# Performance work log

Hardware: AMD Instinct MI355X
Metric: run time of the kernel (lower is better)

## Reference

```python
import jax, jax.numpy as jnp
import numpy as np

EPS = 1e-6


def _make_window_masks(nhw, nww, ws, shift):
    ph = jnp.arange(nhw).reshape(nhw, 1, 1, 1, 1, 1)
    pw = jnp.arange(nww).reshape(1, nww, 1, 1, 1, 1)
    qh = jnp.arange(ws).reshape(1, 1, ws, 1, 1, 1)
    qw = jnp.arange(ws).reshape(1, 1, 1, ws, 1, 1)
    kh = jnp.arange(ws).reshape(1, 1, 1, 1, ws, 1)
    kw = jnp.arange(ws).reshape(1, 1, 1, 1, 1, ws)
    top = ph == 0
    left = pw == 0
    qa = qh < shift
    ka = kh < shift
    ql = qw < shift
    kl = kw < shift
    m = ((left & top & (ql == kl) & (qa == ka))
         | (left & ~top & (ql == kl))
         | (~left & top & (qa == ka))
         | (~left & ~top))
    m = jnp.broadcast_to(m, (nhw, nww, ws, ws, ws, ws))
    return m.reshape(nhw, nww, ws * ws, ws * ws)


def _window(ws, x):
    # x: [b, nh, H, W, e] -> [b, nh, H//ws, W//ws, ws, ws, e]
    b, nh, H, W, e = x.shape
    x = x.reshape(b, nh, H // ws, ws, W // ws, ws, e)
    return jnp.transpose(x, (0, 1, 2, 4, 3, 5, 6))


def _unwindow(x):
    b, nh, h, w, wh, ww, e = x.shape
    x = jnp.transpose(x, (0, 1, 2, 4, 3, 5, 6))
    return x.reshape(b, nh, h * wh, w * ww, e)


def _rope_theta(pos, n_heads, d_head):
    # AxialRoPE: dim = d_head // 2, freqs [n_heads, dim//4]
    dim = d_head // 2
    freqs = jnp.exp(jnp.linspace(np.float32(np.log(np.pi)), np.float32(np.log(10.0 * np.pi)), n_heads * dim // 4 + 1)[:-1])
    freqs = freqs.reshape(dim // 4, n_heads).T  # [nh, dim//4]
    th = pos[..., None, 0:1] * freqs  # [b,H,W,nh,dim//4]
    tw = pos[..., None, 1:2] * freqs
    theta = jnp.concatenate([th, tw], axis=-1)  # [b,H,W,nh,d_head//4]
    return jnp.moveaxis(theta, -2, -4)  # [b,nh,H,W,d_head//4]


def _apply_rope(x, theta):
    # rotates first 2*d of head dim, pairs (i, i+d); rest passes through
    d = theta.shape[-1]
    x1, x2, rest = x[..., :d], x[..., d:2 * d], x[..., 2 * d:]
    cos, sin = jnp.cos(theta), jnp.sin(theta)
    y1 = x1 * cos - x2 * sin
    y2 = x2 * cos + x1 * sin
    return jnp.concatenate([y1, y2, rest], axis=-1)


def _forward(x, pos, cond, norm_scale, mod_w, mod_b, qkv_w, attn_scale, out_w, window_size, window_shift):
    b, H, W, d_model = x.shape
    n_heads = attn_scale.shape[0]
    d_head = d_model // n_heads
    ws, shift = window_size, window_shift
    skip = x
    # adaLN modulation: SiLU -> Linear(cond_features, 3*d_model)
    c = jax.nn.silu(cond) @ mod_w.T + mod_b  # [b, 3*d_model]
    sh, sc, gate = jnp.split(c, 3, axis=-1)
    # RMSNorm
    ms = jnp.mean(jnp.square(x.astype(jnp.float32)), axis=-1, keepdims=True)
    xn = x * (norm_scale * jax.lax.rsqrt(ms + EPS)).astype(x.dtype)
    # modulate
    xn = xn * (1.0 + sc[:, None, None, :]) + sh[:, None, None, :]
    # qkv projection: rearrange 'n h w (t nh e) -> t n nh h w e'
    qkv = (xn @ qkv_w.T).reshape(b, H, W, 3, n_heads, d_head)
    qkv = jnp.transpose(qkv, (3, 0, 4, 1, 2, 5))  # [3,b,nh,H,W,e]
    q, k, v = qkv[0], qkv[1], qkv[2]
    # cosine-sim QK scaling (per-head learned scale, eps 1e-6)
    sqrt_s = jnp.sqrt(attn_scale)[:, None, None, None]
    q = q * (sqrt_s * jax.lax.rsqrt(jnp.sum(jnp.square(q), -1, keepdims=True) + EPS))
    k = k * (sqrt_s * jax.lax.rsqrt(jnp.sum(jnp.square(k), -1, keepdims=True) + EPS))
    # axial RoPE
    theta = _rope_theta(pos, n_heads, d_head)
    q = _apply_rope(q, theta)
    k = _apply_rope(k, theta)
    # shifted-window attention with sdpa scale = 1.0
    def shift_win(t):
        return _window(ws, jnp.roll(t, (shift, shift), axis=(-3, -2)))
    h, w = H // ws, W // ws
    L = ws * ws
    qs = shift_win(q).reshape(b, n_heads, h, w, L, d_head)
    ks = shift_win(k).reshape(b, n_heads, h, w, L, d_head)
    vs = shift_win(v).reshape(b, n_heads, h, w, L, d_head)
    mask = _make_window_masks(h, w, ws, shift)  # [h,w,L,L] bool
    scores = jnp.einsum('bnhwqe,bnhwke->bnhwqk', qs, ks)
    scores = jnp.where(mask, scores, jnp.asarray(-1e9, scores.dtype))
    attn = jax.nn.softmax(scores, axis=-1)
    o = jnp.einsum('bnhwqk,bnhwke->bnhwqe', attn, vs)
    o = o.reshape(b, n_heads, h, w, ws, ws, d_head)
    o = jnp.roll(_unwindow(o), (-shift, -shift), axis=(-3, -2))  # [b,nh,H,W,e]
    o = jnp.transpose(o, (0, 2, 3, 1, 4)).reshape(b, H, W, d_model)
    o = o @ out_w.T
    return skip + gate[:, None, None, :] * o


def setup_inputs() -> dict:
    key = jax.random.key(0)
    ks = jax.random.split(key, 6)
    B, H, W, D, NH, CF = 2, 256, 256, 256, 4, 768
    x = jax.random.normal(ks[0], (B, H, W, D), jnp.float32)
    hh = jnp.linspace(-1.0, 1.0, H)
    ww = jnp.linspace(-1.0, 1.0, W)
    pos = jnp.stack(jnp.meshgrid(hh, ww, indexing='ij'), axis=-1)  # [H,W,2]
    pos = jnp.broadcast_to(pos, (B, H, W, 2)).astype(jnp.float32)
    cond = jax.random.normal(ks[1], (B, CF), jnp.float32)
    norm_scale = jnp.ones((D,), jnp.float32)
    mod_w = jax.random.normal(ks[2], (3 * D, CF), jnp.float32) * 0.02
    mod_b = jnp.zeros((3 * D,), jnp.float32)
    qkv_w = jax.random.normal(ks[3], (3 * D, D), jnp.float32) * (D ** -0.5)
    attn_scale = jnp.full((NH,), 10.0, jnp.float32)
    out_w = jax.random.normal(ks[4], (D, D), jnp.float32) * (D ** -0.5)
    return {"x": x, "pos": pos, "cond": cond, "norm_scale": norm_scale,
            "mod_w": mod_w, "mod_b": mod_b, "qkv_w": qkv_w,
            "attn_scale": attn_scale, "out_w": out_w,
            "window_size": 8, "window_shift": 4}


def reference(x, pos, cond, norm_scale, mod_w, mod_b, qkv_w, attn_scale, out_w, window_size, window_shift):
    return _forward(x, pos, cond, norm_scale, mod_w, mod_b, qkv_w, attn_scale, out_w, window_size, window_shift)
```

## Files before the change

### kernel.cpp

```cpp
#include <hip/hip_runtime.h>
#include <hip/hip_bf16.h>
#include <cstdint>

#define DEV __device__ __forceinline__

constexpr int D_   = 256;
constexpr int CF_  = 768;
constexpr int NTOK = 131072;
constexpr int SHIFT = 4;
constexpr float EPS_ = 1e-6f;

typedef short bf16x8 __attribute__((ext_vector_type(8)));
typedef float f32x4  __attribute__((ext_vector_type(4)));

DEV float bf2f(unsigned short u) {
    unsigned v = ((unsigned)u) << 16;
    return __builtin_bit_cast(float, v);
}
DEV unsigned short f2bf(float f) {
    unsigned u = __builtin_bit_cast(unsigned, f);
    unsigned r = (u + 0x7fffu + ((u >> 16) & 1u)) >> 16;
    return (unsigned short)r;
}
DEV unsigned cvtpk(float lo, float hi) {
    unsigned r;
    asm("v_cvt_pk_bf16_f32 %0, %1, %2" : "=v"(r) : "v"(lo), "v"(hi));
    return r;
}
DEV float wave_sum(float v) {
    #pragma unroll
    for (int o = 32; o; o >>= 1) v += __shfl_xor(v, o, 64);
    return v;
}
DEV void gl_lds16(const void* g, void* l) {
    __builtin_amdgcn_global_load_lds(
        (const __attribute__((address_space(1))) void*)g,
        (__attribute__((address_space(3))) void*)l, 16, 0, 0);
}

__global__ void k_mod(const float* __restrict__ cond, const float* __restrict__ mod_w,
                      const float* __restrict__ mod_b, float* __restrict__ c) {
    int wv = threadIdx.x >> 6, lane = threadIdx.x & 63;
    int idx = blockIdx.x * 4 + wv;
    int b = idx / (3 * D_), j = idx % (3 * D_);
    float acc = 0.f;
    for (int k = lane; k < CF_; k += 64) {
        float cv = cond[b * CF_ + k];
        float s = cv / (1.f + expf(-cv));
        acc += s * mod_w[(size_t)j * CF_ + k];
    }
    acc = wave_sum(acc);
    if (lane == 0) c[b * (3 * D_) + j] = acc + mod_b[j];
}

__global__ void k_prep(const float* __restrict__ x, const float* __restrict__ c,
                       const float* __restrict__ norm_scale,
                       const float* __restrict__ qkv_w, const float* __restrict__ out_w,
                       unsigned short* __restrict__ xnb,
                       unsigned short* __restrict__ qkvwb, unsigned short* __restrict__ outwb) {
    if (blockIdx.x < 32768) {
        int wv = threadIdx.x >> 6, lane = threadIdx.x & 63;
        int t = blockIdx.x * 4 + wv;
        int b = t >> 16;
        const float* xp = x + (size_t)t * D_ + lane * 4;
        float4 v = *(const float4*)xp;
        float s = v.x * v.x + v.y * v.y + v.z * v.z + v.w * v.w;
        s = wave_sum(s);
        float rinv = rsqrtf(s * (1.f / D_) + EPS_);
        float4 sc = *(const float4*)(c + b * 768 + 256 + lane * 4);
        float4 sh = *(const float4*)(c + b * 768 + lane * 4);
        float4 ns = *(const float4*)(norm_scale + lane * 4);
        float y0 = v.x * rinv * ((1.f + sc.x) * ns.x) + sh.x;
        float y1 = v.y * rinv * ((1.f + sc.y) * ns.y) + sh.y;
        float y2 = v.z * rinv * ((1.f + sc.z) * ns.z) + sh.z;
        float y3 = v.w * rinv * ((1.f + sc.w) * ns.w) + sh.w;
        uint2 p;
        p.x = cvtpk(y0, y1);
        p.y = cvtpk(y2, y3);
        *(uint2*)(xnb + (size_t)t * D_ + lane * 4) = p;
    } else {
        int i = (blockIdx.x - 32768) * 256 + threadIdx.x;
        const float* src; unsigned short* dst; int off;
        if (i < 49152) { src = qkv_w; dst = qkvwb; off = i * 4; }
        else           { src = out_w; dst = outwb; off = (i - 49152) * 4; }
        float4 v = *(const float4*)(src + off);
        uint2 p;
        p.x = cvtpk(v.x, v.y);
        p.y = cvtpk(v.z, v.w);
        *(uint2*)(dst + off) = p;
    }
}

__global__ __launch_bounds__(256) void k_qkv_mfma(const unsigned short* __restrict__ xnb,
                                                  const unsigned short* __restrict__ wb,
                                                  const float* __restrict__ attn_scale,
                                                  unsigned short* __restrict__ qkv) {
    __shared__ unsigned short As[2][128 * 32];
    __shared__ unsigned short Bs[2][128 * 32];
    const int t = threadIdx.x, l = t & 63, w = t >> 6;
    const int bid = blockIdx.x;
    const int lid = (bid & 7) * 768 + (bid >> 3);
    const int m0 = (lid / 6) * 128;
    const int nt = lid % 6;
    const int n0 = nt * 128;
    const int wm = w >> 1, wn = w & 1;
    f32x4 acc[4][4] = {};

    const int srow = w * 32 + (l >> 2);
    const int scol = (l & 3) * 8;
    const unsigned short* aA = xnb + (size_t)(m0 + srow) * 256 + scol;
    const unsigned short* aB = wb  + (size_t)(n0 + srow) * 256 + scol;

    auto stage = [&](int buf, int k0) {
        gl_lds16(aA + k0,            &As[buf][(w * 2 + 0) * 512]);
        gl_lds16(aA + k0 + 16 * 256, &As[buf][(w * 2 + 1) * 512]);
        gl_lds16(aB + k0,            &Bs[buf][(w * 2 + 0) * 512]);
        gl_lds16(aB + k0 + 16 * 256, &Bs[buf][(w * 2 + 1) * 512]);
    };

    stage(0, 0);
    __syncthreads();
    int cur = 0;
    #pragma unroll
    for (int step = 0; step < 8; ++step) {
        if (step < 7) stage(cur ^ 1, (step + 1) * 32);
        bf16x8 af[4], bff[4];
        #pragma unroll
        for (int i = 0; i < 4; i++) {
            af[i]  = *(const bf16x8*)&As[cur][(wm * 64 + i * 16 + (l & 15)) * 32 + (l >> 4) * 8];
            bff[i] = *(const bf16x8*)&Bs[cur][(wn * 64 + i * 16 + (l & 15)) * 32 + (l >> 4) * 8];
        }
        #pragma unroll
        for (int i = 0; i < 4; i++)
            #pragma unroll
            for (int j = 0; j < 4; j++)
                acc[i][j] = __builtin_amdgcn_mfma_f32_16x16x32_bf16(af[i], bff[j], acc[i][j], 0, 0, 0);
        __syncthreads();
        cur ^= 1;
    }

    const int row0 = m0 + wm * 64 + (l >> 4) * 4;
    const int col0 = n0 + wn * 64 + (l & 15);
    const int q16 = l & 15;

    if (nt < 4) {
        const int head = (nt * 2 + wn) & 3;
        const float ssc = sqrtf(attn_scale[head]);
        const float freq = expf(1.14472988584940017f + (float)((q16 & 7) * 4 + head) * 0.07195578545544534f);
        #pragma unroll
        for (int i = 0; i < 4; i++) {
            #pragma unroll
            for (int rg = 0; rg < 4; rg++) {
                float ss = acc[i][0][rg] * acc[i][0][rg] + acc[i][1][rg] * acc[i][1][rg]
                         + acc[i][2][rg] * acc[i][2][rg] + acc[i][3][rg] * acc[i][3][rg];
                ss += __shfl_xor(ss, 1, 64);
                ss += __shfl_xor(ss, 2, 64);
                ss += __shfl_xor(ss, 4, 64);
                ss += __shfl_xor(ss, 8, 64);
                const float rinv = ssc * rsqrtf(ss + EPS_);
                const int row = row0 + i * 16 + rg;
                const int oy = (row >> 8) & 255, ox = row & 255;
                const float ph = -1.f + (float)oy * (2.f / 255.f);
                const float pw = -1.f + (float)ox * (2.f / 255.f);
                const float th = ((q16 < 8) ? ph : pw) * freq;
                float sn, cs;
                __sincosf(th, &sn, &cs);
                const float n0v = acc[i][0][rg] * rinv;
                const float n1v = acc[i][1][rg] * rinv;
                const float n2v = acc[i][2][rg] * rinv;
                const float n3v = acc[i][3][rg] * rinv;
                unsigned short* qp = qkv + (size_t)row * 768 + col0;
                qp[0]  = f2bf(n0v * cs - n1v * sn);
                qp[16] = f2bf(n1v * cs + n0v * sn);
                qp[32] = f2bf(n2v);
                qp[48] = f2bf(n3v);
            }
        }
    } else {
        #pragma unroll
        for (int i = 0; i < 4; i++)
            #pragma unroll
            for (int j = 0; j < 4; j++) {
                #pragma unroll
                for (int rg = 0; rg < 4; rg++)
                    qkv[(size_t)(row0 + i * 16 + rg) * 768 + col0 + j * 16] = f2bf(acc[i][j][rg]);
            }
    }
}

__global__ __launch_bounds__(256) void k_attn_out(const unsigned short* __restrict__ qkv,
                                                  const unsigned short* __restrict__ outwb,
                                                  const float* __restrict__ x,
                                                  const float* __restrict__ c,
                                                  float* __restrict__ out) {
    __shared__ unsigned short Mem[4 * 64 * 72];
    __shared__ float Ls[4][64];
    const int w = threadIdx.x >> 6, l = threadIdx.x & 63;
    const int bid = blockIdx.x;
    const int lid = (bid & 7) * 256 + (bid >> 3);
    const int wx = lid & 31, wy = (lid >> 5) & 31, b = lid >> 10;
    const int head = w;
    const int g = l >> 4, q16 = l & 15;
    unsigned short* Vt = &Mem[w * 4608];

    auto tokof = [&](int p) -> size_t {
        int oy = (wy * 8 + (p >> 3) - SHIFT) & 255;
        int ox = (wx * 8 + (p & 7) - SHIFT) & 255;
        return (size_t)b * 65536 + (size_t)oy * 256 + ox;
    };

    {
        const unsigned short* vp = qkv + tokof(l) * 768 + 512 + head * 64;
        uint4 vr[8];
        #pragma unroll
        for (int i = 0; i < 8; i++) vr[i] = *(const uint4*)(vp + i * 8);
        #pragma unroll
        for (int i = 0; i < 8; i++) {
            unsigned wd[4] = {vr[i].x, vr[i].y, vr[i].z, vr[i].w};
            #pragma unroll
            for (int cc = 0; cc < 4; cc++) {
                Vt[(i * 8 + cc * 2 + 0) * 72 + l] = (unsigned short)(wd[cc] & 0xffff);
                Vt[(i * 8 + cc * 2 + 1) * 72 + l] = (unsigned short)(wd[cc] >> 16);
            }
        }
    }

    bf16x8 af[4][2], bq[4][2];
    #pragma unroll
    for (int i = 0; i < 4; i++) {
        size_t tk = tokof(i * 16 + q16);
        const unsigned short* kp = qkv + tk * 768 + 256 + head * 64 + g * 8;
        af[i][0] = *(const bf16x8*)(kp);
        af[i][1] = *(const bf16x8*)(kp + 32);
        const unsigned short* qp = qkv + tk * 768 + head * 64 + g * 8;
        bq[i][0] = *(const bf16x8*)(qp);
        bq[i][1] = *(const bf16x8*)(qp + 32);
    }

    f32x4 st[4][4] = {};
    #pragma unroll
    for (int ks = 0; ks < 2; ks++)
        #pragma unroll
        for (int i = 0; i < 4; i++)
            #pragma unroll
            for (int j = 0; j < 4; j++)
                st[i][j] = __builtin_amdgcn_mfma_f32_16x16x32_bf16(af[i][ks], bq[j][ks], st[i][j], 0, 0, 0);

    const bool topw = (wy == 0), leftw = (wx == 0);
    if (topw || leftw) {
        #pragma unroll
        for (int j = 0; j < 4; j++) {
            int query = 16 * j + q16;
            bool qa = ((query >> 3) < 4), qlf = ((query & 7) < 4);
            #pragma unroll
            for (int i = 0; i < 4; i++)
                #pragma unroll
                for (int r = 0; r < 4; r++) {
                    int key = 16 * i + 4 * g + r;
                    bool ok = (!leftw || (qlf == ((key & 7) < 4))) &&
                              (!topw || (qa == ((key >> 3) < 4)));
                    if (!ok) st[i][j][r] = -1e9f;
                }
        }
    }

    #pragma unroll
    for (int j = 0; j < 4; j++) {
        float m = -1e30f;
        #pragma unroll
        for (int i = 0; i < 4; i++)
            #pragma unroll
            for (int r = 0; r < 4; r++) m = fmaxf(m, st[i][j][r]);
        m = fmaxf(m, __shfl_xor(m, 16, 64));
        m = fmaxf(m, __shfl_xor(m, 32, 64));
        float s = 0.f;
        #pragma unroll
        for (int i = 0; i < 4; i++)
            #pragma unroll
            for (int r = 0; r < 4; r++) {
                float p = __expf(st[i][j][r] - m);
                st[i][j][r] = p;
                s += p;
            }
        s += __shfl_xor(s, 16, 64);
        s += __shfl_xor(s, 32, 64);
        if (g == 0) Ls[w][16 * j + q16] = s;
    }
    __syncthreads();

    bf16x8 vb[4][2];
    #pragma unroll
    for (int j = 0; j < 4; j++) {
        vb[j][0] = *(const bf16x8*)&Vt[(16 * j + q16) * 72 + g * 8];
        vb[j][1] = *(const bf16x8*)&Vt[(16 * j + q16) * 72 + 32 + g * 8];
    }
    const int ghi = g >> 1;
    const int srcl0 = ((2 * (g & 1)) & 3) * 16 + q16;
    const int srcl1 = ((2 * (g & 1) + 1) & 3) * 16 + q16;
    f32x4 o[4][4] = {};
    #pragma unroll
    for (int qb = 0; qb < 4; qb++) {
        unsigned pk[8];
        #pragma unroll
        for (int ih = 0; ih < 4; ih++) {
            pk[2 * ih]     = cvtpk(st[ih][qb][0], st[ih][qb][1]);
            pk[2 * ih + 1] = cvtpk(st[ih][qb][2], st[ih][qb][3]);
        }
        unsigned pw[8];
        #pragma unroll
        for (int ks = 0; ks < 2; ks++) {
            #pragma unroll
            for (int wd = 0; wd < 4; wd++) {
                const int srcl = (wd < 2) ? srcl0 : srcl1;
                unsigned va  = (unsigned)__shfl((int)pk[4 * ks + (wd & 1)], srcl, 64);
                unsigned vbb = (unsigned)__shfl((int)pk[4 * ks + 2 + (wd & 1)], srcl, 64);
                pw[ks * 4 + wd] = ghi ? vbb : va;
            }
        }
        uint4 paw0 = {pw[0], pw[1], pw[2], pw[3]};
        uint4 paw1 = {pw[4], pw[5], pw[6], pw[7]};
        bf16x8 paA = __builtin_bit_cast(bf16x8, paw0);
        bf16x8 paB = __builtin_bit_cast(bf16x8, paw1);
        #pragma unroll
        for (int j = 0; j < 4; j++) {
            o[qb][j] = __builtin_amdgcn_mfma_f32_16x16x32_bf16(paA, vb[j][0], o[qb][j], 0, 0, 0);
            o[qb][j] = __builtin_amdgcn_mfma_f32_16x16x32_bf16(paB, vb[j][1], o[qb][j], 0, 0, 0);
        }
    }

    __syncthreads();
    unsigned short* ost = Mem;
    #pragma unroll
    for (int i = 0; i < 4; i++) {
        float4 lv = *(const float4*)&Ls[w][16 * i + 4 * g];
        float lvr[4] = {lv.x, lv.y, lv.z, lv.w};
        #pragma unroll
        for (int r = 0; r < 4; r++) {
            const float invl = 1.f / lvr[r];
            const int row = 16 * i + 4 * g + r;
            #pragma unroll
            for (int j = 0; j < 4; j++)
                ost[row * 264 + head * 64 + 16 * j + q16] = f2bf(o[i][j][r] * invl);
        }
    }
    __syncthreads();

    f32x4 acc2[4][4] = {};
    #pragma unroll
    for (int ks = 0; ks < 8; ks++) {
        bf16x8 a2[4], b2[4];
        #pragma unroll
        for (int i = 0; i < 4; i++)
            a2[i] = *(const bf16x8*)&ost[(16 * i + q16) * 264 + ks * 32 + g * 8];
        #pragma unroll
        for (int j = 0; j < 4; j++)
            b2[j] = *(const bf16x8*)&outwb[(size_t)(w * 64 + 16 * j + q16) * 256 + ks * 32 + g * 8];
        #pragma unroll
        for (int i = 0; i < 4; i++)
            #pragma unroll
            for (int j = 0; j < 4; j++)
                acc2[i][j] = __builtin_amdgcn_mfma_f32_16x16x32_bf16(a2[i], b2[j], acc2[i][j], 0, 0, 0);
    }

    float gates[4];
    #pragma unroll
    for (int j = 0; j < 4; j++) gates[j] = c[b * 768 + 512 + w * 64 + 16 * j + q16];
    #pragma unroll
    for (int i = 0; i < 4; i++) {
        #pragma unroll
        for (int r = 0; r < 4; r++) {
            const int row = 16 * i + 4 * g + r;
            const size_t tok = tokof(row);
            float* op = out + tok * 256 + w * 64 + q16;
            const float* xp = x + tok * 256 + w * 64 + q16;
            #pragma unroll
            for (int j = 0; j < 4; j++)
                op[16 * j] = xp[16 * j] + gates[j] * acc2[i][j][r];
        }
    }
}

extern "C" void kernel_launch(void* const* d_in, const int* in_sizes, int n_in,
                              void* d_out, int out_size, void* d_ws, size_t ws_size,
                              hipStream_t stream) {
    const float* x          = (const float*)d_in[0];
    const float* cond       = (const float*)d_in[2];
    const float* norm_scale = (const float*)d_in[3];
    const float* mod_w      = (const float*)d_in[4];
    const float* mod_b      = (const float*)d_in[5];
    const float* qkv_w      = (const float*)d_in[6];
    const float* attn_scale = (const float*)d_in[7];
    const float* out_w      = (const float*)d_in[8];

    char* ws = (char*)d_ws;
    float* c               = (float*)ws;
    unsigned short* xnb    = (unsigned short*)(ws + 8192);
    unsigned short* qkvwb  = (unsigned short*)(ws + 8192 + 67108864);
    unsigned short* outwb  = (unsigned short*)(ws + 8192 + 67108864 + 393216);
    unsigned short* qkv    = (unsigned short*)(ws + 8192 + 67108864 + 524288);
    float* out             = (float*)d_out;

    hipLaunchKernelGGL(k_mod,  dim3(384),   dim3(256), 0, stream, cond, mod_w, mod_b, c);
    hipLaunchKernelGGL(k_prep, dim3(33024), dim3(256), 0, stream,
                       x, c, norm_scale, qkv_w, out_w, xnb, qkvwb, outwb);
    hipLaunchKernelGGL(k_qkv_mfma, dim3(6144), dim3(256), 0, stream, xnb, qkvwb, attn_scale, qkv);
    hipLaunchKernelGGL(k_attn_out, dim3(2048), dim3(256), 0, stream, qkv, outwb, x, c, out);
}
```

Baseline: 286.2 us.

## Swizzle QKV GEMM LDS tiles and stage epilogue through LDS for coalesced stores

The QKV GEMM kernel now XOR-swizzles the k-column slot of its LDS A/B tiles, on both the global-to-LDS staging side and the fragment read side, to reduce bank conflicts. The epilogue no longer writes scattered 2-byte bf16 values straight to global memory. It writes the 128x128 output tile into a padded LDS buffer, synchronises, and then each thread stores 16-byte vectors along contiguous rows. The goal is to turn uncoalesced global writes into full-width stores, at the cost of an extra barrier and a larger LDS allocation that may reduce occupancy.

```diff
diff --git a/kernel.cpp b/kernel.cpp
--- a/kernel.cpp
+++ b/kernel.cpp
@@ -95,8 +95,9 @@
                                                   const unsigned short* __restrict__ wb,
                                                   const float* __restrict__ attn_scale,
                                                   unsigned short* __restrict__ qkv) {
-    __shared__ unsigned short As[2][128 * 32];
-    __shared__ unsigned short Bs[2][128 * 32];
+    __shared__ unsigned short SM[17408];
+    unsigned short* As = SM;
+    unsigned short* Bs = SM + 8192;
     const int t = threadIdx.x, l = t & 63, w = t >> 6;
     const int bid = blockIdx.x;
     const int lid = (bid & 7) * 768 + (bid >> 3);
@@ -107,16 +108,19 @@
     f32x4 acc[4][4] = {};
 
     const int srow = w * 32 + (l >> 2);
-    const int scol = (l & 3) * 8;
+    const int scol = (((l & 3) ^ ((l >> 3) & 3)) * 8);
     const unsigned short* aA = xnb + (size_t)(m0 + srow) * 256 + scol;
     const unsigned short* aB = wb  + (size_t)(n0 + srow) * 256 + scol;
 
     auto stage = [&](int buf, int k0) {
-        gl_lds16(aA + k0,            &As[buf][(w * 2 + 0) * 512]);
-        gl_lds16(aA + k0 + 16 * 256, &As[buf][(w * 2 + 1) * 512]);
-        gl_lds16(aB + k0,            &Bs[buf][(w * 2 + 0) * 512]);
-        gl_lds16(aB + k0 + 16 * 256, &Bs[buf][(w * 2 + 1) * 512]);
+        gl_lds16(aA + k0,            &As[buf * 4096 + (w * 2 + 0) * 512]);
+        gl_lds16(aA + k0 + 16 * 256, &As[buf * 4096 + (w * 2 + 1) * 512]);
+        gl_lds16(aB + k0,            &Bs[buf * 4096 + (w * 2 + 0) * 512]);
+        gl_lds16(aB + k0 + 16 * 256, &Bs[buf * 4096 + (w * 2 + 1) * 512]);
     };
+
+    const int q16 = l & 15, g = l >> 4;
+    const int rslot = (g ^ ((q16 >> 1) & 3)) * 8;
 
     stage(0, 0);
     __syncthreads();
@@ -127,8 +131,8 @@
         bf16x8 af[4], bff[4];
         #pragma unroll
         for (int i = 0; i < 4; i++) {
-            af[i]  = *(const bf16x8*)&As[cur][(wm * 64 + i * 16 + (l & 15)) * 32 + (l >> 4) * 8];
-            bff[i] = *(const bf16x8*)&Bs[cur][(wn * 64 + i * 16 + (l & 15)) * 32 + (l >> 4) * 8];
+            af[i]  = *(const bf16x8*)&As[cur * 4096 + (wm * 64 + i * 16 + q16) * 32 + rslot];
+            bff[i] = *(const bf16x8*)&Bs[cur * 4096 + (wn * 64 + i * 16 + q16) * 32 + rslot];
         }
         #pragma unroll
         for (int i = 0; i < 4; i++)
@@ -139,9 +143,8 @@
         cur ^= 1;
     }
 
-    const int row0 = m0 + wm * 64 + (l >> 4) * 4;
-    const int col0 = n0 + wn * 64 + (l & 15);
-    const int q16 = l & 15;
+    const int rl0 = wm * 64 + g * 4;
+    const int cl0 = wn * 64 + q16;
 
     if (nt < 4) {
         const int head = (nt * 2 + wn) & 3;
@@ -158,7 +161,8 @@
                 ss += __shfl_xor(ss, 4, 64);
                 ss += __shfl_xor(ss, 8, 64);
                 const float rinv = ssc * rsqrtf(ss + EPS_);
-                const int row = row0 + i * 16 + rg;
+                const int rl = rl0 + i * 16 + rg;
+                const int row = m0 + rl;
                 const int oy = (row >> 8) & 255, ox = row & 255;
                 const float ph = -1.f + (float)oy * (2.f / 255.f);
                 const float pw = -1.f + (float)ox * (2.f / 255.f);
@@ -169,22 +173,33 @@
                 const float n1v = acc[i][1][rg] * rinv;
                 const float n2v = acc[i][2][rg] * rinv;
                 const float n3v = acc[i][3][rg] * rinv;
-                unsigned short* qp = qkv + (size_t)row * 768 + col0;
-                qp[0]  = f2bf(n0v * cs - n1v * sn);
-                qp[16] = f2bf(n1v * cs + n0v * sn);
-                qp[32] = f2bf(n2v);
-                qp[48] = f2bf(n3v);
+                SM[rl * 136 + cl0]      = f2bf(n0v * cs - n1v * sn);
+                SM[rl * 136 + cl0 + 16] = f2bf(n1v * cs + n0v * sn);
+                SM[rl * 136 + cl0 + 32] = f2bf(n2v);
+                SM[rl * 136 + cl0 + 48] = f2bf(n3v);
             }
         }
     } else {
         #pragma unroll
         for (int i = 0; i < 4; i++)
             #pragma unroll
-            for (int j = 0; j < 4; j++) {
+            for (int rg = 0; rg < 4; rg++) {
+                const int rl = rl0 + i * 16 + rg;
                 #pragma unroll
-                for (int rg = 0; rg < 4; rg++)
-                    qkv[(size_t)(row0 + i * 16 + rg) * 768 + col0 + j * 16] = f2bf(acc[i][j][rg]);
+                for (int j = 0; j < 4; j++)
+                    SM[rl * 136 + cl0 + j * 16] = f2bf(acc[i][j][rg]);
             }
+    }
+    __syncthreads();
+
+    {
+        const int cr = (t & 15) * 8, rr = t >> 4;
+        #pragma unroll
+        for (int it = 0; it < 8; it++) {
+            const int rl = rr + it * 16;
+            uint4 vv = *(const uint4*)&SM[rl * 136 + cr];
+            *(uint4*)(qkv + (size_t)(m0 + rl) * 768 + n0 + cr) = vv;
+        }
     }
 }
 
```

Result: faster. 260.9 us (-8.8%).
